# Kernel optimization log

Hardware: AMD Instinct MI355X
Metric: run time of the kernel (lower is better)

The kernel has to match this reference:

```python
import jax, jax.numpy as jnp
import numpy as np

EMB = 768
BLOCK = 64
K = EMB // BLOCK  # 12


def setup_inputs() -> dict:
    key = jax.random.key(0)
    ks = jax.random.split(key, 8)
    n, c, d, h, E, M, P = 4, 1024, 768, 12, 32, 4, 256
    seq = jax.random.normal(ks[0], (n, c, d), dtype=jnp.float32)
    attn = jax.random.uniform(ks[1], (n, h, c, c), dtype=jnp.float32)
    attn = attn / attn.sum(-1, keepdims=True)  # attention-like rows
    mention_pos = jax.random.randint(ks[2], (n, E, M), 0, c)
    hts = jax.random.randint(ks[3], (n, P, 2), 0, E)
    W_head = jax.random.normal(ks[4], (2 * d, EMB), dtype=jnp.float32) / np.sqrt(2 * d)
    W_tail = jax.random.normal(ks[5], (2 * d, EMB), dtype=jnp.float32) / np.sqrt(2 * d)
    W_bil = jax.random.normal(ks[6], (EMB * BLOCK, 97), dtype=jnp.float32) / np.sqrt(EMB * BLOCK)
    return {
        "sequence_output": seq,
        "attention": attn,
        "mention_pos": mention_pos,
        "hts": hts,
        "W_head": W_head,
        "b_head": jnp.zeros((EMB,), jnp.float32),
        "W_tail": W_tail,
        "b_tail": jnp.zeros((EMB,), jnp.float32),
        "W_bil": W_bil,
        "b_bil": jnp.zeros((97,), jnp.float32),
    }


def reference(sequence_output, attention, mention_pos, hts,
              W_head, b_head, W_tail, b_tail, W_bil, b_bil):
    n, c, d = sequence_output.shape
    h = attention.shape[1]
    P = hts.shape[1]

    bidx = jnp.arange(n)[:, None, None]
    # gather mention token embeddings: [n, E, M, d]
    m_emb = sequence_output[bidx, mention_pos]
    # entity embedding = logsumexp over mentions (single-mention case is identical)
    ent_emb = jax.nn.logsumexp(m_emb, axis=2)                      # [n, E, d]

    # per-mention attention rows: attention[i, :, pos, :] -> [n, E, M, h, c]
    att_t = jnp.transpose(attention, (0, 2, 1, 3))                 # [n, c, h, c]
    m_att = att_t[bidx, mention_pos]                               # [n, E, M, h, c]
    ent_att = m_att.mean(axis=2)                                   # [n, E, h, c]

    pidx = jnp.arange(n)[:, None]
    hs = ent_emb[pidx, hts[..., 0]]                                # [n, P, d]
    ts = ent_emb[pidx, hts[..., 1]]
    h_att = ent_att[pidx, hts[..., 0]]                             # [n, P, h, c]
    t_att = ent_att[pidx, hts[..., 1]]

    ht_att = (h_att * t_att).mean(axis=2)                          # [n, P, c]
    ht_att = ht_att / (ht_att.sum(-1, keepdims=True) + 1e-30)
    # relation context: contract('ld,rl->rd') per doc
    rs = jnp.einsum('ncd,npc->npd', sequence_output, ht_att)       # [n, P, d]

    R = n * P
    hs2 = jnp.tanh(jnp.concatenate([hs, rs], -1).reshape(R, 2 * d) @ W_head + b_head)
    ts2 = jnp.tanh(jnp.concatenate([ts, rs], -1).reshape(R, 2 * d) @ W_tail + b_tail)

    b1 = hs2.reshape(R, K, BLOCK)
    b2 = ts2.reshape(R, K, BLOCK)
    bl = (b1[:, :, :, None] * b2[:, :, None, :]).reshape(R, EMB * BLOCK)
    logits = bl @ W_bil + b_bil                                    # [R, 97]
    return logits
```

## Files before the change

kernel.cpp:

```cpp
#include <hip/hip_runtime.h>
#include <hip/hip_bf16.h>
#include <math.h>

#define ND 4
#define CL 1024
#define DD 768
#define HH 12
#define EE 32
#define MMEN 4
#define PP 256
#define EMBD 768
#define KBL 12
#define OUTD 97
#define RTOT (ND*PP)

typedef unsigned short u16;
typedef __attribute__((ext_vector_type(8))) short short8;
typedef __attribute__((ext_vector_type(4))) float f32x4;

static __device__ inline float bf16u_to_f(unsigned v){
  union { unsigned u; float f; } c; c.u = v << 16; return c.f;
}
static __device__ inline unsigned f_to_bf16u(float f){
  union { float f; unsigned u; } c; c.f = f;
  return (c.u + 0x7fffu + ((c.u >> 16) & 1u)) >> 16;
}

#define GLOAD_LDS16(gp, lp) __builtin_amdgcn_global_load_lds( \
    (const __attribute__((address_space(1))) unsigned*)(gp), \
    (__attribute__((address_space(3))) unsigned*)(lp), 16, 0, 0)

__global__ __launch_bounds__(256) void k_ent_emb(const float* __restrict__ seq,
    const int* __restrict__ mpos, u16* __restrict__ ent_emb_bf)
{
  int idx = blockIdx.x*256 + threadIdx.x;
  if (idx >= ND*EE*DD) return;
  int dd = idx % DD;
  int e  = (idx / DD) % EE;
  int i  = idx / (DD*EE);
  const int* mp = mpos + (i*EE + e)*MMEN;
  float v[MMEN];
  float mx = -1e30f;
  #pragma unroll
  for (int m=0;m<MMEN;m++){
    v[m] = seq[(i*CL + mp[m])*DD + dd];
    mx = fmaxf(mx, v[m]);
  }
  float s = 0.f;
  #pragma unroll
  for (int m=0;m<MMEN;m++) s += expf(v[m]-mx);
  ent_emb_bf[idx] = (u16)f_to_bf16u(mx + logf(s));
}

__global__ __launch_bounds__(256) void k_ent_att(const float* __restrict__ attn,
    const int* __restrict__ mpos, float* __restrict__ ent_att)
{
  int idx = blockIdx.x*256 + threadIdx.x;
  if (idx >= ND*EE*HH*CL) return;
  int j    = idx % CL;
  int head = (idx / CL) % HH;
  int e    = (idx / (CL*HH)) % EE;
  int i    = idx / (CL*HH*EE);
  const int* mp = mpos + (i*EE + e)*MMEN;
  float s = 0.f;
  #pragma unroll
  for (int m=0;m<MMEN;m++)
    s += attn[((size_t)(i*HH + head)*CL + mp[m])*CL + j];
  ent_att[idx] = s * (1.f/MMEN);
}

__global__ __launch_bounds__(256) void k_ht_att(const float* __restrict__ ent_att,
    const int* __restrict__ hts, u16* __restrict__ ht_att_bf)
{
  int bp = blockIdx.x;
  int i  = bp / PP;
  int tid = threadIdx.x;
  int he = hts[bp*2+0];
  int te = hts[bp*2+1];
  const float* ha = ent_att + ((size_t)(i*EE + he)*HH)*CL;
  const float* ta = ent_att + ((size_t)(i*EE + te)*HH)*CL;
  float v[4];
  #pragma unroll
  for (int q=0;q<4;q++){
    int j = tid + q*256;
    float s = 0.f;
    #pragma unroll
    for (int head=0; head<HH; head++)
      s += ha[head*CL + j] * ta[head*CL + j];
    v[q] = s * (1.f/HH);
  }
  float part = v[0]+v[1]+v[2]+v[3];
  #pragma unroll
  for (int off=32; off>0; off>>=1) part += __shfl_down(part, off, 64);
  __shared__ float wsum[4];
  __shared__ float tot_s;
  int lane = tid & 63, wv = tid >> 6;
  if (lane==0) wsum[wv] = part;
  __syncthreads();
  if (tid==0) tot_s = wsum[0]+wsum[1]+wsum[2]+wsum[3];
  __syncthreads();
  float inv = 1.f/(tot_s + 1e-30f);
  #pragma unroll
  for (int q=0;q<4;q++){
    int j = tid + q*256;
    ht_att_bf[(size_t)bp*CL + j] = (u16)f_to_bf16u(v[q]*inv);
  }
}

__global__ __launch_bounds__(256) void k_transpose_bf(const float* __restrict__ src,
    u16* __restrict__ dst, int R, int C)
{
  size_t boff = (size_t)blockIdx.z * R * C;
  src += boff; dst += boff;
  __shared__ float t[32][33];
  int tx = threadIdx.x & 31, ty = threadIdx.x >> 5;
  int c0 = blockIdx.x*32, r0 = blockIdx.y*32;
  #pragma unroll
  for (int q=0;q<4;q++)
    t[ty+8*q][tx] = src[(size_t)(r0+ty+8*q)*C + c0+tx];
  __syncthreads();
  #pragma unroll
  for (int q=0;q<4;q++)
    dst[(size_t)(c0+ty+8*q)*R + r0+tx] = (u16)f_to_bf16u(t[tx][ty+8*q]);
}

__global__ __launch_bounds__(256) void k_gemm_rs_mfma(
    const u16* __restrict__ ht_att_bf, const u16* __restrict__ seq_t_bf,
    u16* __restrict__ rs_bf)
{
  const int rt = blockIdx.x, ct = blockIdx.y, doc = blockIdx.z;
  const u16* A  = ht_att_bf + (size_t)doc*PP*CL;
  const u16* Bt = seq_t_bf  + (size_t)doc*DD*CL;
  const int row0 = rt*128, col0 = ct*64;
  __shared__ __align__(16) u16 As[128*32];
  __shared__ __align__(16) u16 Bs[64*32];
  const int tid = threadIdx.x, lane = tid & 63, wave = tid >> 6;
  const int m = lane & 15, j8 = lane >> 4;
  const int srow = lane >> 2, schunk = lane & 3;
  f32x4 acc[2][4];
  #pragma unroll
  for (int a=0;a<2;a++)
    #pragma unroll
    for (int b=0;b<4;b++) acc[a][b] = (f32x4){0.f,0.f,0.f,0.f};

  for (int k0 = 0; k0 < CL; k0 += 32){
    __syncthreads();
    #pragma unroll
    for (int ii=0; ii<2; ii++){
      int i = wave*2 + ii;
      int row = i*16 + srow;
      int gc = schunk ^ ((row>>1)&3);
      const u16* gp = A + (size_t)(row0+row)*CL + k0 + gc*8;
      GLOAD_LDS16(gp, &As[i*16*32]);
    }
    {
      int row = wave*16 + srow;
      int gc = schunk ^ ((row>>1)&3);
      const u16* gp = Bt + (size_t)(col0+row)*CL + k0 + gc*8;
      GLOAD_LDS16(gp, &Bs[wave*16*32]);
    }
    __syncthreads();
    short8 af[2], bf[4];
    #pragma unroll
    for (int mf=0; mf<2; mf++){
      int r = wave*32 + mf*16 + m;
      af[mf] = *(const short8*)&As[r*32 + 8*(j8 ^ ((r>>1)&3))];
    }
    #pragma unroll
    for (int nt=0; nt<4; nt++){
      int n = nt*16 + m;
      bf[nt] = *(const short8*)&Bs[n*32 + 8*(j8 ^ ((n>>1)&3))];
    }
    #pragma unroll
    for (int mf=0; mf<2; mf++)
      #pragma unroll
      for (int nt=0; nt<4; nt++)
        acc[mf][nt] = __builtin_amdgcn_mfma_f32_16x16x32_bf16(af[mf], bf[nt], acc[mf][nt], 0,0,0);
  }

  #pragma unroll
  for (int mf=0; mf<2; mf++){
    #pragma unroll
    for (int nt=0; nt<4; nt++){
      int colg = col0 + nt*16 + m;
      #pragma unroll
      for (int reg=0; reg<4; reg++){
        int rowg = doc*PP + row0 + wave*32 + mf*16 + j8*4 + reg;
        rs_bf[(size_t)rowg*DD + colg] = (u16)f_to_bf16u(acc[mf][nt][reg]);
      }
    }
  }
}

__global__ __launch_bounds__(256) void k_prepare_ab(
    const u16* __restrict__ ent_emb_bf, const u16* __restrict__ rs_bf,
    const int* __restrict__ hts, uint4* __restrict__ Ah, uint4* __restrict__ At)
{
  int idx = blockIdx.x*256 + threadIdx.x;
  if (idx >= RTOT*192) return;
  int g = idx % 192, r = idx / 192;
  int doc = r >> 8;
  int he = hts[r*2+0], te = hts[r*2+1];
  uint4 vh, vt;
  if (g < 96){
    vh = ((const uint4*)ent_emb_bf)[(size_t)(doc*EE+he)*96 + g];
    vt = ((const uint4*)ent_emb_bf)[(size_t)(doc*EE+te)*96 + g];
  } else {
    uint4 v = ((const uint4*)rs_bf)[(size_t)r*96 + (g-96)];
    vh = v; vt = v;
  }
  Ah[idx] = vh; At[idx] = vt;
}

__global__ __launch_bounds__(256) void k_gemm_ht_mfma(
    const u16* __restrict__ Ah, const u16* __restrict__ At,
    const u16* __restrict__ Wht, const u16* __restrict__ Wtt,
    const float* __restrict__ b_head, const float* __restrict__ b_tail,
    float* __restrict__ hs2, float* __restrict__ ts2)
{
  const int rt = blockIdx.x, ct = blockIdx.y, z = blockIdx.z;
  const u16* A    = z ? At  : Ah;
  const u16* Bt   = z ? Wtt : Wht;
  const float* bias = z ? b_tail : b_head;
  float* C        = z ? ts2 : hs2;
  const int row0 = rt*128, col0 = ct*64;
  __shared__ __align__(16) u16 As[128*32];
  __shared__ __align__(16) u16 Bs[64*32];
  const int tid = threadIdx.x, lane = tid & 63, wave = tid >> 6;
  const int m = lane & 15, j8 = lane >> 4;
  const int srow = lane >> 2, schunk = lane & 3;
  f32x4 acc[2][4];
  #pragma unroll
  for (int a=0;a<2;a++)
    #pragma unroll
    for (int b=0;b<4;b++) acc[a][b] = (f32x4){0.f,0.f,0.f,0.f};

  for (int k0 = 0; k0 < 1536; k0 += 32){
    __syncthreads();
    #pragma unroll
    for (int ii=0; ii<2; ii++){
      int i = wave*2 + ii;
      int row = i*16 + srow;
      int gc = schunk ^ ((row>>1)&3);
      const u16* gp = A + (size_t)(row0+row)*1536 + k0 + gc*8;
      GLOAD_LDS16(gp, &As[i*16*32]);
    }
    {
      int row = wave*16 + srow;
      int gc = schunk ^ ((row>>1)&3);
      const u16* gp = Bt + (size_t)(col0+row)*1536 + k0 + gc*8;
      GLOAD_LDS16(gp, &Bs[wave*16*32]);
    }
    __syncthreads();
    short8 af[2], bf[4];
    #pragma unroll
    for (int mf=0; mf<2; mf++){
      int r = wave*32 + mf*16 + m;
      af[mf] = *(const short8*)&As[r*32 + 8*(j8 ^ ((r>>1)&3))];
    }
    #pragma unroll
    for (int nt=0; nt<4; nt++){
      int n = nt*16 + m;
      bf[nt] = *(const short8*)&Bs[n*32 + 8*(j8 ^ ((n>>1)&3))];
    }
    #pragma unroll
    for (int mf=0; mf<2; mf++)
      #pragma unroll
      for (int nt=0; nt<4; nt++)
        acc[mf][nt] = __builtin_amdgcn_mfma_f32_16x16x32_bf16(af[mf], bf[nt], acc[mf][nt], 0,0,0);
  }

  #pragma unroll
  for (int mf=0; mf<2; mf++){
    #pragma unroll
    for (int nt=0; nt<4; nt++){
      int colg = col0 + nt*16 + m;
      float bv = bias[colg];
      #pragma unroll
      for (int reg=0; reg<4; reg++){
        int rowg = row0 + wave*32 + mf*16 + j8*4 + reg;
        C[(size_t)rowg*DD + colg] = tanhf(acc[mf][nt][reg] + bv);
      }
    }
  }
}

__global__ __launch_bounds__(256) void k_wt2(const float* __restrict__ W_bil,
    u16* __restrict__ Wt2)
{
  const int cc = blockIdx.x;
  __shared__ u16 lds2[4480];
  int tid = threadIdx.x;
  for (int u=tid; u<4480; u+=256) lds2[u] = 0;
  __syncthreads();
  for (int u=tid; u<112*32; u+=256){
    int kk = u / 112, n = u % 112;
    if (n < OUTD)
      lds2[n*40 + kk] = (u16)f_to_bf16u(W_bil[(size_t)(cc*32 + kk)*OUTD + n]);
  }
  __syncthreads();
  uint4* dst = (uint4*)(Wt2 + (size_t)cc*4480);
  const uint4* src = (const uint4*)lds2;
  for (int v=tid; v<560; v+=256) dst[v] = src[v];
}

__global__ __launch_bounds__(256) void k_init_logits(const float* __restrict__ b_bil,
    float* __restrict__ out)
{
  int idx = blockIdx.x*256 + threadIdx.x;
  if (idx >= RTOT*OUTD) return;
  out[idx] = b_bil[idx % OUTD];
}

__global__ __launch_bounds__(256) void k_bilinear(
    const float* __restrict__ hs2, const float* __restrict__ ts2,
    const u16* __restrict__ Wt2, float* __restrict__ logits)
{
  const int rt = blockIdx.x;
  const int sp = blockIdx.y;
  const int kb = sp >> 2;
  const int i0 = (sp & 3) * 16;
  const int row0 = rt * 128;

  __shared__ __align__(16) float b1s[128][17];
  __shared__ __align__(16) u16 b2s[128][72];
  __shared__ __align__(16) u16 Ws[4480];

  const int tid = threadIdx.x;
  const int lane = tid & 63, wave = tid >> 6;
  const int m = lane & 15, j8 = lane >> 4;

  for (int u=tid; u<128*16; u+=256){
    int r = u >> 4, ii = u & 15;
    b1s[r][ii] = hs2[(size_t)(row0+r)*EMBD + kb*64 + i0 + ii];
  }
  for (int u=tid; u<128*64; u+=256){
    int r = u >> 6, j = u & 63;
    b2s[r][j] = (u16)f_to_bf16u(ts2[(size_t)(row0+r)*EMBD + kb*64 + j]);
  }

  const uint4* gsrc = (const uint4*)(Wt2 + (size_t)(sp*32)*4480);
  uint4* ws4 = (uint4*)Ws;
  uint4 pf0, pf1, pf2;
  {
    pf0 = gsrc[tid];
    pf1 = gsrc[tid+256];
    if (tid < 48) pf2 = gsrc[tid+512];
  }

  f32x4 acc[2][7];
  #pragma unroll
  for (int f=0;f<2;f++)
    #pragma unroll
    for (int nt=0;nt<7;nt++) acc[f][nt] = (f32x4){0.f,0.f,0.f,0.f};

  for (int c=0; c<32; c++){
    __syncthreads();
    ws4[tid] = pf0; ws4[tid+256] = pf1; if (tid < 48) ws4[tid+512] = pf2;
    if (c+1 < 32){
      size_t b = (size_t)(c+1)*560;
      pf0 = gsrc[b+tid];
      pf1 = gsrc[b+tid+256];
      if (tid < 48) pf2 = gsrc[b+tid+512];
    }
    __syncthreads();

    const int i_rel = c >> 1;
    const int j0 = (c & 1) * 32;

    short8 bfr[7];
    #pragma unroll
    for (int nt=0;nt<7;nt++)
      bfr[nt] = *(const short8*)&Ws[(nt*16 + m)*40 + j8*8];

    #pragma unroll
    for (int f=0;f<2;f++){
      int r = wave*32 + f*16 + m;
      float s = b1s[r][i_rel];
      uint4 u = *(const uint4*)&b2s[r][j0 + j8*8];
      unsigned uw[4] = {u.x, u.y, u.z, u.w};
      short8 af;
      #pragma unroll
      for (int e=0;e<4;e++){
        af[2*e]   = (short)f_to_bf16u(s * bf16u_to_f(uw[e] & 0xffffu));
        af[2*e+1] = (short)f_to_bf16u(s * bf16u_to_f(uw[e] >> 16));
      }
      #pragma unroll
      for (int nt=0;nt<7;nt++)
        acc[f][nt] = __builtin_amdgcn_mfma_f32_16x16x32_bf16(af, bfr[nt], acc[f][nt], 0, 0, 0);
    }
  }

  #pragma unroll
  for (int f=0;f<2;f++){
    #pragma unroll
    for (int nt=0;nt<7;nt++){
      int col = nt*16 + m;
      if (col < OUTD){
        #pragma unroll
        for (int reg=0;reg<4;reg++){
          int grow = row0 + wave*32 + f*16 + j8*4 + reg;
          atomicAdd(&logits[(size_t)grow*OUTD + col], acc[f][nt][reg]);
        }
      }
    }
  }
}

extern "C" void kernel_launch(void* const* d_in, const int* in_sizes, int n_in,
                              void* d_out, int out_size, void* d_ws, size_t ws_size,
                              hipStream_t stream)
{
  const float* seq    = (const float*)d_in[0];
  const float* attn   = (const float*)d_in[1];
  const int*   mpos   = (const int*)d_in[2];
  const int*   hts    = (const int*)d_in[3];
  const float* W_head = (const float*)d_in[4];
  const float* b_head = (const float*)d_in[5];
  const float* W_tail = (const float*)d_in[6];
  const float* b_tail = (const float*)d_in[7];
  const float* W_bil  = (const float*)d_in[8];
  const float* b_bil  = (const float*)d_in[9];
  float* logits = (float*)d_out;

  float* ws = (float*)d_ws;
  u16*   ent_emb_bf = (u16*)(ws + 0);
  u16*   rs_bf      = (u16*)(ws + 49152);
  float* hs2        = ws + 442368;
  float* ts2        = ws + 1228800;
  u16*   Wh_t       = (u16*)(ws + 2015232);
  u16*   Wt_t       = (u16*)(ws + 2605056);
  u16*   Ah_bf      = (u16*)(ws + 3194880);
  u16*   At_bf      = (u16*)(ws + 3981312);
  float* ent_att    = ws + 4767744;
  u16*   seq_t_bf   = (u16*)(ws + 6340608);
  u16*   ht_att_bf  = (u16*)(ws + 7913472);
  u16*   Wt2        = (u16*)(ws + 4767744);

  k_ent_emb<<<(ND*EE*DD+255)/256, 256, 0, stream>>>(seq, mpos, ent_emb_bf);
  k_ent_att<<<(ND*EE*HH*CL+255)/256, 256, 0, stream>>>(attn, mpos, ent_att);
  k_ht_att<<<ND*PP, 256, 0, stream>>>(ent_att, hts, ht_att_bf);
  k_transpose_bf<<<dim3(DD/32, CL/32, ND), 256, 0, stream>>>(seq, seq_t_bf, CL, DD);
  k_transpose_bf<<<dim3(DD/32, 1536/32, 1), 256, 0, stream>>>(W_head, Wh_t, 1536, DD);
  k_transpose_bf<<<dim3(DD/32, 1536/32, 1), 256, 0, stream>>>(W_tail, Wt_t, 1536, DD);
  k_gemm_rs_mfma<<<dim3(2, 12, 4), 256, 0, stream>>>(ht_att_bf, seq_t_bf, rs_bf);
  k_prepare_ab<<<(RTOT*192+255)/256, 256, 0, stream>>>(ent_emb_bf, rs_bf, hts,
      (uint4*)Ah_bf, (uint4*)At_bf);
  k_gemm_ht_mfma<<<dim3(8, 12, 2), 256, 0, stream>>>(Ah_bf, At_bf, Wh_t, Wt_t,
      b_head, b_tail, hs2, ts2);
  k_wt2<<<1536, 256, 0, stream>>>(W_bil, Wt2);
  k_init_logits<<<(RTOT*OUTD+255)/256, 256, 0, stream>>>(b_bil, logits);
  k_bilinear<<<dim3(RTOT/128, 48), 256, 0, stream>>>(hs2, ts2, Wt2, logits);
}
```

Before: 404.6 us.

## Replace atomic split-K accumulation with partial buffer and reduction kernel

The bilinear kernel now writes each split's partial logits to a dedicated workspace slice instead of issuing float atomicAdds into the output, and a new reduction kernel sums the 48 slices and adds the bias. This removes the separate logits-initialization kernel and the atomic contention from many blocks updating the same outputs. The two weight transposes are also merged into one launch. The cost is extra global traffic, since roughly 48×1024×112 floats are written and then read back, plus one more kernel launch.

Result: faster. 377.4 us (-6.7%).

```diff
diff --git a/kernel.cpp b/kernel.cpp
--- a/kernel.cpp
+++ b/kernel.cpp
@@ -13,6 +13,7 @@
 #define KBL 12
 #define OUTD 97
 #define RTOT (ND*PP)
+#define NSPLIT 48
 
 typedef unsigned short u16;
 typedef __attribute__((ext_vector_type(8))) short short8;
@@ -112,6 +113,24 @@
 {
   size_t boff = (size_t)blockIdx.z * R * C;
   src += boff; dst += boff;
+  __shared__ float t[32][33];
+  int tx = threadIdx.x & 31, ty = threadIdx.x >> 5;
+  int c0 = blockIdx.x*32, r0 = blockIdx.y*32;
+  #pragma unroll
+  for (int q=0;q<4;q++)
+    t[ty+8*q][tx] = src[(size_t)(r0+ty+8*q)*C + c0+tx];
+  __syncthreads();
+  #pragma unroll
+  for (int q=0;q<4;q++)
+    dst[(size_t)(c0+ty+8*q)*R + r0+tx] = (u16)f_to_bf16u(t[tx][ty+8*q]);
+}
+
+__global__ __launch_bounds__(256) void k_transpose_bf_w(
+    const float* __restrict__ srcA, u16* __restrict__ dstA,
+    const float* __restrict__ srcB, u16* __restrict__ dstB, int R, int C)
+{
+  const float* src = blockIdx.z ? srcB : srcA;
+  u16* dst         = blockIdx.z ? dstB : dstA;
   __shared__ float t[32][33];
   int tx = threadIdx.x & 31, ty = threadIdx.x >> 5;
   int c0 = blockIdx.x*32, r0 = blockIdx.y*32;
@@ -304,17 +323,9 @@
   for (int v=tid; v<560; v+=256) dst[v] = src[v];
 }
 
-__global__ __launch_bounds__(256) void k_init_logits(const float* __restrict__ b_bil,
-    float* __restrict__ out)
-{
-  int idx = blockIdx.x*256 + threadIdx.x;
-  if (idx >= RTOT*OUTD) return;
-  out[idx] = b_bil[idx % OUTD];
-}
-
 __global__ __launch_bounds__(256) void k_bilinear(
     const float* __restrict__ hs2, const float* __restrict__ ts2,
-    const u16* __restrict__ Wt2, float* __restrict__ logits)
+    const u16* __restrict__ Wt2, float* __restrict__ pbuf)
 {
   const int rt = blockIdx.x;
   const int sp = blockIdx.y;
@@ -391,20 +402,39 @@
     }
   }
 
+  float* dst = pbuf + ((size_t)sp*RTOT + row0)*112;
   #pragma unroll
   for (int f=0;f<2;f++){
     #pragma unroll
     for (int nt=0;nt<7;nt++){
       int col = nt*16 + m;
-      if (col < OUTD){
-        #pragma unroll
-        for (int reg=0;reg<4;reg++){
-          int grow = row0 + wave*32 + f*16 + j8*4 + reg;
-          atomicAdd(&logits[(size_t)grow*OUTD + col], acc[f][nt][reg]);
-        }
+      #pragma unroll
+      for (int reg=0;reg<4;reg++){
+        int lrow = wave*32 + f*16 + j8*4 + reg;
+        dst[(size_t)lrow*112 + col] = acc[f][nt][reg];
       }
     }
   }
+}
+
+__global__ __launch_bounds__(256) void k_reduce_logits(
+    const float* __restrict__ pbuf, const float* __restrict__ b_bil,
+    float* __restrict__ logits)
+{
+  int idx = blockIdx.x*256 + threadIdx.x;
+  if (idx >= RTOT*112) return;
+  int col = idx % 112, row = idx / 112;
+  if (col >= OUTD) return;
+  float s0 = 0.f, s1 = 0.f, s2 = 0.f, s3 = 0.f;
+  const size_t stride = (size_t)RTOT*112;
+  #pragma unroll
+  for (int sp=0; sp<NSPLIT; sp+=4){
+    s0 += pbuf[(sp+0)*stride + idx];
+    s1 += pbuf[(sp+1)*stride + idx];
+    s2 += pbuf[(sp+2)*stride + idx];
+    s3 += pbuf[(sp+3)*stride + idx];
+  }
+  logits[(size_t)row*OUTD + col] = (s0+s1) + (s2+s3) + b_bil[col];
 }
 
 extern "C" void kernel_launch(void* const* d_in, const int* in_sizes, int n_in,
@@ -436,19 +466,20 @@
   u16*   seq_t_bf   = (u16*)(ws + 6340608);
   u16*   ht_att_bf  = (u16*)(ws + 7913472);
   u16*   Wt2        = (u16*)(ws + 4767744);
+  float* pbuf       = ws + 8437760;
 
   k_ent_emb<<<(ND*EE*DD+255)/256, 256, 0, stream>>>(seq, mpos, ent_emb_bf);
   k_ent_att<<<(ND*EE*HH*CL+255)/256, 256, 0, stream>>>(attn, mpos, ent_att);
   k_ht_att<<<ND*PP, 256, 0, stream>>>(ent_att, hts, ht_att_bf);
   k_transpose_bf<<<dim3(DD/32, CL/32, ND), 256, 0, stream>>>(seq, seq_t_bf, CL, DD);
-  k_transpose_bf<<<dim3(DD/32, 1536/32, 1), 256, 0, stream>>>(W_head, Wh_t, 1536, DD);
-  k_transpose_bf<<<dim3(DD/32, 1536/32, 1), 256, 0, stream>>>(W_tail, Wt_t, 1536, DD);
+  k_transpose_bf_w<<<dim3(DD/32, 1536/32, 2), 256, 0, stream>>>(
+      W_head, Wh_t, W_tail, Wt_t, 1536, DD);
   k_gemm_rs_mfma<<<dim3(2, 12, 4), 256, 0, stream>>>(ht_att_bf, seq_t_bf, rs_bf);
   k_prepare_ab<<<(RTOT*192+255)/256, 256, 0, stream>>>(ent_emb_bf, rs_bf, hts,
       (uint4*)Ah_bf, (uint4*)At_bf);
   k_gemm_ht_mfma<<<dim3(8, 12, 2), 256, 0, stream>>>(Ah_bf, At_bf, Wh_t, Wt_t,
       b_head, b_tail, hs2, ts2);
   k_wt2<<<1536, 256, 0, stream>>>(W_bil, Wt2);
-  k_init_logits<<<(RTOT*OUTD+255)/256, 256, 0, stream>>>(b_bil, logits);
-  k_bilinear<<<dim3(RTOT/128, 48), 256, 0, stream>>>(hs2, ts2, Wt2, logits);
-}
+  k_bilinear<<<dim3(RTOT/128, NSPLIT), 256, 0, stream>>>(hs2, ts2, Wt2, pbuf);
+  k_reduce_logits<<<(RTOT*112+255)/256, 256, 0, stream>>>(pbuf, b_bil, logits);
+}
```
